# Performance work log

Measured on AMD Instinct MI355X. Metric: run time of the kernel, lower is better.

## Reference

```python
import jax, jax.numpy as jnp
import numpy as np
import math

D_PAIR = 64
N_HEADS = 4
D_HEAD = D_PAIR // N_HEADS


def setup_inputs() -> dict:
    key = jax.random.key(0)
    ks = jax.random.split(key, 9)
    B, L, D = 2, 256, D_PAIR
    s = 1.0 / math.sqrt(D)
    return {
        "z": jax.random.normal(ks[0], (B, L, L, D), dtype=jnp.float32),
        "ln_scale": jnp.ones((D,), jnp.float32),
        "ln_bias": jnp.zeros((D,), jnp.float32),
        "Wq": jax.random.normal(ks[1], (D, D), jnp.float32) * s,
        "Wk": jax.random.normal(ks[2], (D, D), jnp.float32) * s,
        "Wv": jax.random.normal(ks[3], (D, D), jnp.float32) * s,
        "Wg": jax.random.normal(ks[4], (D, D), jnp.float32) * s,
        "bg": jax.random.normal(ks[5], (D,), jnp.float32) * 0.02,
        "Wo": jax.random.normal(ks[6], (D, D), jnp.float32) * s,
        "bo": jax.random.normal(ks[7], (D,), jnp.float32) * 0.02,
    }


def _layernorm(x, scale, bias, eps=1e-5):
    mu = jnp.mean(x, axis=-1, keepdims=True)
    var = jnp.var(x, axis=-1, keepdims=True)
    return (x - mu) * jax.lax.rsqrt(var + eps) * scale + bias


def reference(z, ln_scale, ln_bias, Wq, Wk, Wv, Wg, bg, Wo, bo):
    B, L, _, D = z.shape
    H, Dh = N_HEADS, D_HEAD
    zn = _layernorm(z, ln_scale, ln_bias)
    # torch Linear(no bias): x @ W.T
    Q = (zn @ Wq.T).reshape(B, L, L, H, Dh)
    K = (zn @ Wk.T).reshape(B, L, L, H, Dh)
    V = (zn @ Wv.T).reshape(B, L, L, H, Dh)
    scale = 1.0 / math.sqrt(Dh)
    # row-wise attention: for each row l, attend over column index j
    attn = jnp.einsum("blihd,bljhd->blhij", Q, K) * scale  # [B,L,H,L,L]
    attn = jax.nn.softmax(attn, axis=-1)
    out = jnp.einsum("blhij,bljhd->blihd", attn, V).reshape(B, L, L, D)
    gate = jax.nn.sigmoid(zn @ Wg.T + bg)
    out = gate * out
    return out @ Wo.T + bo
```

## Files before the change

kernel.cpp:

```cpp
#include <hip/hip_runtime.h>
#include <math.h>


typedef __attribute__((ext_vector_type(4))) float f32x4;
typedef __attribute__((ext_vector_type(8))) short s16x8;

#define MFMA16(a, b, c) __builtin_amdgcn_mfma_f32_16x16x32_bf16((a), (b), (c), 0, 0, 0)

__device__ __forceinline__ short f2bf(float x) {
    union { float f; unsigned u; } v; v.f = x;
    unsigned r = v.u + 0x7fffu + ((v.u >> 16) & 1u);
    return (short)(r >> 16);
}
__device__ __forceinline__ s16x8 cvt8(const float* p) {
    s16x8 r;
    #pragma unroll
    for (int u = 0; u < 8; ++u) r[u] = f2bf(p[u]);
    return r;
}

static constexpr int VSTRIDE = 264;
static constexpr int PS = 40;

__global__ __launch_bounds__(256, 2)
void ka_fused(const float* __restrict__ z, const float* __restrict__ ln_s,
              const float* __restrict__ ln_b, const float* __restrict__ Wq,
              const float* __restrict__ Wk, const float* __restrict__ Wv,
              const float* __restrict__ Wg, const float* __restrict__ bg,
              short* __restrict__ ws)
{
    __shared__ __align__(16) short znl[256 * 64];
    __shared__ __align__(16) short Ksh[256 * 16];
    __shared__ __align__(16) short Vt[16 * VSTRIDE];
    __shared__ __align__(16) short rpb[4][64 * PS];

    const int tid = threadIdx.x, lane = tid & 63, w = tid >> 6;
    const int n16 = lane & 15, quad = lane >> 4;
    const bool qlo = (quad < 2);
    const int g = blockIdx.x, bl = g >> 2, h = g & 3;
    const size_t rowbase = (size_t)bl * (256 * 64);
    short* rp = rpb[w];

    {
        float zn[64];
        const float4* zp4 = (const float4*)(z + rowbase + (size_t)tid * 64);
        #pragma unroll
        for (int gq = 0; gq < 16; ++gq) {
            float4 v4 = zp4[gq];
            zn[gq * 4 + 0] = v4.x; zn[gq * 4 + 1] = v4.y;
            zn[gq * 4 + 2] = v4.z; zn[gq * 4 + 3] = v4.w;
        }
        float mu = 0.f;
        #pragma unroll
        for (int k = 0; k < 64; ++k) mu += zn[k];
        mu *= (1.f / 64.f);
        float va = 0.f;
        #pragma unroll
        for (int k = 0; k < 64; ++k) { float d = zn[k] - mu; va += d * d; }
        const float rs = rsqrtf(va * (1.f / 64.f) + 1e-5f);
        #pragma unroll
        for (int k = 0; k < 64; ++k) zn[k] = (zn[k] - mu) * rs * ln_s[k] + ln_b[k];
        #pragma unroll
        for (int gq = 0; gq < 8; ++gq) {
            s16x8 v;
            #pragma unroll
            for (int u = 0; u < 8; ++u) v[u] = f2bf(zn[gq * 8 + u]);
            *(s16x8*)&znl[tid * 64 + ((gq ^ (tid & 7)) * 8)] = v;
        }
    }

    s16x8 bfr[4][2];
    {
        const float* Wt0 = Wq; const float* Wt1 = Wk;
        const float* Wt2 = Wv; const float* Wt3 = Wg;
        #pragma unroll
        for (int ks = 0; ks < 2; ++ks) {
            size_t off = (size_t)(h * 16 + n16) * 64 + ks * 32 + quad * 8;
            bfr[0][ks] = cvt8(Wt0 + off);
            bfr[1][ks] = cvt8(Wt1 + off);
            bfr[2][ks] = cvt8(Wt2 + off);
            bfr[3][ks] = cvt8(Wt3 + off);
        }
    }
    const float bgv = bg[h * 16 + n16];

    f32x4 g4[4];
    #pragma unroll
    for (int mt = 0; mt < 4; ++mt) {
        const int row = w * 64 + mt * 16 + n16;
        s16x8 a0 = *(const s16x8*)&znl[row * 64 + ((quad ^ (n16 & 7)) * 8)];
        s16x8 a1 = *(const s16x8*)&znl[row * 64 + (((4 + quad) ^ (n16 & 7)) * 8)];
        f32x4 aq = {}, ak = {}, av = {}, ag = {};
        aq = MFMA16(a0, bfr[0][0], aq); aq = MFMA16(a1, bfr[0][1], aq);
        ak = MFMA16(a0, bfr[1][0], ak); ak = MFMA16(a1, bfr[1][1], ak);
        av = MFMA16(a0, bfr[2][0], av); av = MFMA16(a1, bfr[2][1], av);
        ag = MFMA16(a0, bfr[3][0], ag); ag = MFMA16(a1, bfr[3][1], ag);
        #pragma unroll
        for (int r = 0; r < 4; ++r)
            rp[(mt * 16 + quad * 4 + r) * PS + n16] = f2bf(0.25f * aq[r]);
        #pragma unroll
        for (int r = 0; r < 4; ++r) {
            int pos = w * 64 + mt * 16 + quad * 4 + r;
            Ksh[pos * 16 + (((n16 >> 3) ^ (pos & 1)) * 8) + (n16 & 7)] = f2bf(ak[r]);
        }
        {
            unsigned lo = (unsigned)(unsigned short)f2bf(av[0]) |
                          ((unsigned)(unsigned short)f2bf(av[1]) << 16);
            unsigned hi = (unsigned)(unsigned short)f2bf(av[2]) |
                          ((unsigned)(unsigned short)f2bf(av[3]) << 16);
            uint2 pk = {lo, hi};
            *(uint2*)&Vt[n16 * VSTRIDE + w * 64 + mt * 16 + quad * 4] = pk;
        }
        #pragma unroll
        for (int r = 0; r < 4; ++r)
            g4[mt][r] = 1.f / (1.f + __expf(-(ag[r] + bgv)));
    }

    s16x8 qa[4];
    #pragma unroll
    for (int mt = 0; mt < 4; ++mt) {
        s16x8 q = {};
        if (qlo) q = *(const s16x8*)&rp[(mt * 16 + n16) * PS + quad * 8];
        qa[mt] = q;
    }
    __syncthreads();

    float lrow[4][4];
    f32x4 o4[4];
    #pragma unroll
    for (int mt = 0; mt < 4; ++mt) {
        o4[mt] = {};
        #pragma unroll
        for (int r = 0; r < 4; ++r) lrow[mt][r] = 0.f;
    }
    for (int ch = 0; ch < 8; ++ch) {
        #pragma unroll
        for (int jtl = 0; jtl < 2; ++jtl) {
            int j = ch * 32 + jtl * 16 + n16;
            s16x8 kf = {};
            if (qlo) kf = *(const s16x8*)&Ksh[j * 16 + ((quad ^ (j & 1)) * 8)];
            int jc = jtl * 16 + n16, jb = jc >> 3;
            #pragma unroll
            for (int mt = 0; mt < 4; ++mt) {
                f32x4 zc = {};
                f32x4 s = MFMA16(qa[mt], kf, zc);
                #pragma unroll
                for (int r = 0; r < 4; ++r) {
                    float e = __expf(s[r]);
                    lrow[mt][r] += e;
                    int rin = mt * 16 + quad * 4 + r;
                    rp[rin * PS + ((jb ^ (rin & 3)) * 8) + (jc & 7)] = f2bf(e);
                }
            }
        }
        #pragma unroll
        for (int mt = 0; mt < 4; ++mt) {
            int rin = mt * 16 + n16;
            s16x8 pa = *(const s16x8*)&rp[rin * PS + ((quad ^ (rin & 3)) * 8)];
            s16x8 vf = *(const s16x8*)&Vt[n16 * VSTRIDE + ch * 32 + quad * 8];
            o4[mt] = MFMA16(pa, vf, o4[mt]);
        }
    }
    #pragma unroll
    for (int d = 1; d < 16; d <<= 1)
        #pragma unroll
        for (int mt = 0; mt < 4; ++mt)
            #pragma unroll
            for (int r = 0; r < 4; ++r)
                lrow[mt][r] += __shfl_xor(lrow[mt][r], d);

    #pragma unroll
    for (int mt = 0; mt < 4; ++mt)
        #pragma unroll
        for (int r = 0; r < 4; ++r) {
            float go = g4[mt][r] * o4[mt][r] / lrow[mt][r];
            rp[(mt * 16 + quad * 4 + r) * PS + n16] = f2bf(go);
        }
    {
        s16x8 p0 = *(const s16x8*)&rp[lane * PS];
        s16x8 p1 = *(const s16x8*)&rp[lane * PS + 8];
        short* dst = ws + (((size_t)h * 512 + bl) * 256 + w * 64 + lane) * 16;
        *(s16x8*)&dst[0] = p0;
        *(s16x8*)&dst[8] = p1;
    }
}

__global__ __launch_bounds__(256, 4)
void k3_out(const short* __restrict__ ws, const float* __restrict__ Wo,
            const float* __restrict__ bo, float* __restrict__ out)
{
    const int tid = threadIdx.x, lane = tid & 63, w = tid >> 6;
    const int n16 = lane & 15, quad = lane >> 4;
    const short* GO = ws;
    const int bl = blockIdx.x;
    const int rowloc = w * 64;

    s16x8 bfr[4][2];
    #pragma unroll
    for (int nt = 0; nt < 4; ++nt)
        #pragma unroll
        for (int ks = 0; ks < 2; ++ks)
            bfr[nt][ks] = cvt8(Wo + (size_t)(nt * 16 + n16) * 64 + ks * 32 + quad * 8);

    f32x4 acc[4][4] = {};
    #pragma unroll
    for (int mt = 0; mt < 4; ++mt) {
        #pragma unroll
        for (int c = 0; c < 2; ++c) {
            int hp = c * 2 + (quad >> 1);
            const short* ap = &GO[(((size_t)hp * 512 + bl) * 256 + rowloc + mt * 16 + n16) * 16
                                  + (quad & 1) * 8];
            s16x8 a = *(const s16x8*)ap;
            #pragma unroll
            for (int nt = 0; nt < 4; ++nt)
                acc[mt][nt] = MFMA16(a, bfr[nt][c], acc[mt][nt]);
        }
    }
    #pragma unroll
    for (int nt = 0; nt < 4; ++nt) {
        float bov = bo[nt * 16 + n16];
        #pragma unroll
        for (int mt = 0; mt < 4; ++mt)
            #pragma unroll
            for (int r = 0; r < 4; ++r)
                out[((size_t)bl * 256 + rowloc + mt * 16 + quad * 4 + r) * 64 + nt * 16 + n16] =
                    acc[mt][nt][r] + bov;
    }
}

extern "C" void kernel_launch(void* const* d_in, const int* in_sizes, int n_in,
                              void* d_out, int out_size, void* d_ws, size_t ws_size,
                              hipStream_t stream) {
    const float* z  = (const float*)d_in[0];
    const float* ls = (const float*)d_in[1];
    const float* lb = (const float*)d_in[2];
    const float* Wq = (const float*)d_in[3];
    const float* Wk = (const float*)d_in[4];
    const float* Wv = (const float*)d_in[5];
    const float* Wg = (const float*)d_in[6];
    const float* bg = (const float*)d_in[7];
    const float* Wo = (const float*)d_in[8];
    const float* bo = (const float*)d_in[9];
    float* out = (float*)d_out;
    short* wsp = (short*)d_ws;

    hipLaunchKernelGGL(ka_fused, dim3(2048), dim3(256), 0, stream,
                       z, ls, lb, Wq, Wk, Wv, Wg, bg, wsp);
    hipLaunchKernelGGL(k3_out, dim3(512), dim3(256), 0, stream, wsp, Wo, bo, out);
}
```

Baseline: 174.9 us.

## Alias attention LDS buffers, transpose MFMA operands, use exp2 and packed bf16 conversion

Shared memory is merged into one buffer. The per-wave probability and Q staging reuse the LayerNorm tile region, which cuts LDS per block so three blocks fit per CU instead of two. The Q/K/gate MFMAs are transposed so that scores come out in a key-major layout. That makes the row sum mostly a per-lane reduction needing two shuffles, and lets the P stores be packed 64-bit writes. Softmax uses exp2 with log2(e) folded into the Q scale, bf16 conversion uses the hardware packed intrinsic, and the output projection kernel runs twice as many smaller blocks. The risks are register pressure under the tighter launch bound and new bank-conflict patterns from the changed swizzles.

```diff
diff --git a/kernel.cpp b/kernel.cpp
--- a/kernel.cpp
+++ b/kernel.cpp
@@ -1,4 +1,5 @@
 #include <hip/hip_runtime.h>
+#include <hip/hip_bf16.h>
 #include <math.h>
 
 
@@ -7,39 +8,38 @@
 
 #define MFMA16(a, b, c) __builtin_amdgcn_mfma_f32_16x16x32_bf16((a), (b), (c), 0, 0, 0)
 
-__device__ __forceinline__ short f2bf(float x) {
-    union { float f; unsigned u; } v; v.f = x;
-    unsigned r = v.u + 0x7fffu + ((v.u >> 16) & 1u);
-    return (short)(r >> 16);
+__device__ __forceinline__ unsigned pk2(float a, float b) {
+    union { __hip_bfloat162 h; unsigned u; } c;
+    float2 t; t.x = a; t.y = b;
+    c.h = __float22bfloat162_rn(t);
+    return c.u;
 }
 __device__ __forceinline__ s16x8 cvt8(const float* p) {
-    s16x8 r;
-    #pragma unroll
-    for (int u = 0; u < 8; ++u) r[u] = f2bf(p[u]);
-    return r;
-}
-
-static constexpr int VSTRIDE = 264;
-static constexpr int PS = 40;
-
-__global__ __launch_bounds__(256, 2)
+    union { unsigned u[4]; s16x8 v; } r;
+    r.u[0] = pk2(p[0], p[1]); r.u[1] = pk2(p[2], p[3]);
+    r.u[2] = pk2(p[4], p[5]); r.u[3] = pk2(p[6], p[7]);
+    return r.v;
+}
+
+static constexpr int ZNL = 0;
+static constexpr int KSH = 16384;
+static constexpr int VT  = 20480;
+static constexpr int LDS_EL = 24704;
+
+__global__ __launch_bounds__(256, 3)
 void ka_fused(const float* __restrict__ z, const float* __restrict__ ln_s,
               const float* __restrict__ ln_b, const float* __restrict__ Wq,
               const float* __restrict__ Wk, const float* __restrict__ Wv,
               const float* __restrict__ Wg, const float* __restrict__ bg,
               short* __restrict__ ws)
 {
-    __shared__ __align__(16) short znl[256 * 64];
-    __shared__ __align__(16) short Ksh[256 * 16];
-    __shared__ __align__(16) short Vt[16 * VSTRIDE];
-    __shared__ __align__(16) short rpb[4][64 * PS];
-
+    __shared__ __align__(16) short lds[LDS_EL];
     const int tid = threadIdx.x, lane = tid & 63, w = tid >> 6;
     const int n16 = lane & 15, quad = lane >> 4;
     const bool qlo = (quad < 2);
     const int g = blockIdx.x, bl = g >> 2, h = g & 3;
     const size_t rowbase = (size_t)bl * (256 * 64);
-    short* rp = rpb[w];
+    const int wsl = w * 4096;
 
     {
         float zn[64];
@@ -60,128 +60,118 @@
         const float rs = rsqrtf(va * (1.f / 64.f) + 1e-5f);
         #pragma unroll
         for (int k = 0; k < 64; ++k) zn[k] = (zn[k] - mu) * rs * ln_s[k] + ln_b[k];
+        const int lr = lane;
         #pragma unroll
         for (int gq = 0; gq < 8; ++gq) {
-            s16x8 v;
-            #pragma unroll
-            for (int u = 0; u < 8; ++u) v[u] = f2bf(zn[gq * 8 + u]);
-            *(s16x8*)&znl[tid * 64 + ((gq ^ (tid & 7)) * 8)] = v;
-        }
-    }
-
-    s16x8 bfr[4][2];
-    {
-        const float* Wt0 = Wq; const float* Wt1 = Wk;
-        const float* Wt2 = Wv; const float* Wt3 = Wg;
-        #pragma unroll
-        for (int ks = 0; ks < 2; ++ks) {
-            size_t off = (size_t)(h * 16 + n16) * 64 + ks * 32 + quad * 8;
-            bfr[0][ks] = cvt8(Wt0 + off);
-            bfr[1][ks] = cvt8(Wt1 + off);
-            bfr[2][ks] = cvt8(Wt2 + off);
-            bfr[3][ks] = cvt8(Wt3 + off);
-        }
-    }
-    const float bgv = bg[h * 16 + n16];
-
-    f32x4 g4[4];
-    #pragma unroll
-    for (int mt = 0; mt < 4; ++mt) {
-        const int row = w * 64 + mt * 16 + n16;
-        s16x8 a0 = *(const s16x8*)&znl[row * 64 + ((quad ^ (n16 & 7)) * 8)];
-        s16x8 a1 = *(const s16x8*)&znl[row * 64 + (((4 + quad) ^ (n16 & 7)) * 8)];
+            union { unsigned u[4]; s16x8 v; } pkv;
+            pkv.u[0] = pk2(zn[gq * 8 + 0], zn[gq * 8 + 1]);
+            pkv.u[1] = pk2(zn[gq * 8 + 2], zn[gq * 8 + 3]);
+            pkv.u[2] = pk2(zn[gq * 8 + 4], zn[gq * 8 + 5]);
+            pkv.u[3] = pk2(zn[gq * 8 + 6], zn[gq * 8 + 7]);
+            *(s16x8*)&lds[ZNL + wsl + (lr >> 4) * 1024 + (lr & 15) * 64
+                          + ((gq ^ (lr & 7)) * 8)] = pkv.v;
+        }
+    }
+
+    s16x8 bq[2], bk[2], bv[2], bgf[2];
+    #pragma unroll
+    for (int ks = 0; ks < 2; ++ks) {
+        size_t off = (size_t)(h * 16 + n16) * 64 + ks * 32 + quad * 8;
+        bq[ks] = cvt8(Wq + off);  bk[ks] = cvt8(Wk + off);
+        bv[ks] = cvt8(Wv + off);  bgf[ks] = cvt8(Wg + off);
+    }
+    const float4 bg4 = *(const float4*)(bg + h * 16 + quad * 4);
+    constexpr float QS = 0.25f * 1.44269504088896340736f;
+
+    float g4t[4][4];
+    #pragma unroll
+    for (int t = 0; t < 4; ++t) {
+        s16x8 zn0 = *(const s16x8*)&lds[ZNL + wsl + t * 1024 + n16 * 64
+                                        + ((quad ^ (n16 & 7)) * 8)];
+        s16x8 zn1 = *(const s16x8*)&lds[ZNL + wsl + t * 1024 + n16 * 64
+                                        + (((4 + quad) ^ (n16 & 7)) * 8)];
         f32x4 aq = {}, ak = {}, av = {}, ag = {};
-        aq = MFMA16(a0, bfr[0][0], aq); aq = MFMA16(a1, bfr[0][1], aq);
-        ak = MFMA16(a0, bfr[1][0], ak); ak = MFMA16(a1, bfr[1][1], ak);
-        av = MFMA16(a0, bfr[2][0], av); av = MFMA16(a1, bfr[2][1], av);
-        ag = MFMA16(a0, bfr[3][0], ag); ag = MFMA16(a1, bfr[3][1], ag);
+        aq = MFMA16(bq[0], zn0, aq);  aq = MFMA16(bq[1], zn1, aq);
+        ak = MFMA16(bk[0], zn0, ak);  ak = MFMA16(bk[1], zn1, ak);
+        ag = MFMA16(bgf[0], zn0, ag); ag = MFMA16(bgf[1], zn1, ag);
+        av = MFMA16(zn0, bv[0], av);  av = MFMA16(zn1, bv[1], av);
+        {
+            uint2 p = {pk2(aq[0] * QS, aq[1] * QS), pk2(aq[2] * QS, aq[3] * QS)};
+            *(uint2*)&lds[ZNL + wsl + t * 1024 + n16 * 16 + quad * 4] = p;
+        }
+        {
+            uint2 p = {pk2(ak[0], ak[1]), pk2(ak[2], ak[3])};
+            *(uint2*)&lds[KSH + (w * 64 + t * 16 + n16) * 16 + quad * 4] = p;
+        }
+        {
+            uint2 p = {pk2(av[0], av[1]), pk2(av[2], av[3])};
+            *(uint2*)&lds[VT + n16 * 264 + (w * 64 + t * 16 + quad * 4)] = p;
+        }
         #pragma unroll
         for (int r = 0; r < 4; ++r)
-            rp[(mt * 16 + quad * 4 + r) * PS + n16] = f2bf(0.25f * aq[r]);
-        #pragma unroll
-        for (int r = 0; r < 4; ++r) {
-            int pos = w * 64 + mt * 16 + quad * 4 + r;
-            Ksh[pos * 16 + (((n16 >> 3) ^ (pos & 1)) * 8) + (n16 & 7)] = f2bf(ak[r]);
-        }
-        {
-            unsigned lo = (unsigned)(unsigned short)f2bf(av[0]) |
-                          ((unsigned)(unsigned short)f2bf(av[1]) << 16);
-            unsigned hi = (unsigned)(unsigned short)f2bf(av[2]) |
-                          ((unsigned)(unsigned short)f2bf(av[3]) << 16);
-            uint2 pk = {lo, hi};
-            *(uint2*)&Vt[n16 * VSTRIDE + w * 64 + mt * 16 + quad * 4] = pk;
-        }
-        #pragma unroll
-        for (int r = 0; r < 4; ++r)
-            g4[mt][r] = 1.f / (1.f + __expf(-(ag[r] + bgv)));
+            g4t[t][r] = 1.f / (1.f + __expf(-(ag[r] + bg4[r])));
     }
 
     s16x8 qa[4];
     #pragma unroll
-    for (int mt = 0; mt < 4; ++mt) {
+    for (int qt = 0; qt < 4; ++qt) {
         s16x8 q = {};
-        if (qlo) q = *(const s16x8*)&rp[(mt * 16 + n16) * PS + quad * 8];
-        qa[mt] = q;
+        if (qlo) q = *(const s16x8*)&lds[ZNL + wsl + qt * 1024 + n16 * 16 + quad * 8];
+        qa[qt] = q;
     }
     __syncthreads();
 
     float lrow[4][4];
     f32x4 o4[4];
     #pragma unroll
-    for (int mt = 0; mt < 4; ++mt) {
-        o4[mt] = {};
-        #pragma unroll
-        for (int r = 0; r < 4; ++r) lrow[mt][r] = 0.f;
-    }
+    for (int qt = 0; qt < 4; ++qt) {
+        o4[qt] = {};
+        #pragma unroll
+        for (int r = 0; r < 4; ++r) lrow[qt][r] = 0.f;
+    }
+    const int sw = (n16 ^ (n16 >> 2)) & 3;
     for (int ch = 0; ch < 8; ++ch) {
         #pragma unroll
         for (int jtl = 0; jtl < 2; ++jtl) {
-            int j = ch * 32 + jtl * 16 + n16;
+            int jt = ch * 2 + jtl;
             s16x8 kf = {};
-            if (qlo) kf = *(const s16x8*)&Ksh[j * 16 + ((quad ^ (j & 1)) * 8)];
-            int jc = jtl * 16 + n16, jb = jc >> 3;
+            if (qlo) kf = *(const s16x8*)&lds[KSH + (jt * 16 + n16) * 16 + quad * 8];
+            const int po = (((jtl * 2 + (quad >> 1)) ^ sw) * 8) + (quad & 1) * 4;
             #pragma unroll
-            for (int mt = 0; mt < 4; ++mt) {
+            for (int qt = 0; qt < 4; ++qt) {
                 f32x4 zc = {};
-                f32x4 s = MFMA16(qa[mt], kf, zc);
-                #pragma unroll
-                for (int r = 0; r < 4; ++r) {
-                    float e = __expf(s[r]);
-                    lrow[mt][r] += e;
-                    int rin = mt * 16 + quad * 4 + r;
-                    rp[rin * PS + ((jb ^ (rin & 3)) * 8) + (jc & 7)] = f2bf(e);
-                }
+                f32x4 s = MFMA16(kf, qa[qt], zc);
+                float e0 = exp2f(s[0]), e1 = exp2f(s[1]);
+                float e2 = exp2f(s[2]), e3 = exp2f(s[3]);
+                lrow[qt][0] += e0; lrow[qt][1] += e1;
+                lrow[qt][2] += e2; lrow[qt][3] += e3;
+                uint2 p = {pk2(e0, e1), pk2(e2, e3)};
+                *(uint2*)&lds[ZNL + wsl + qt * 1024 + 256 + n16 * 40 + po] = p;
             }
         }
-        #pragma unroll
-        for (int mt = 0; mt < 4; ++mt) {
-            int rin = mt * 16 + n16;
-            s16x8 pa = *(const s16x8*)&rp[rin * PS + ((quad ^ (rin & 3)) * 8)];
-            s16x8 vf = *(const s16x8*)&Vt[n16 * VSTRIDE + ch * 32 + quad * 8];
-            o4[mt] = MFMA16(pa, vf, o4[mt]);
-        }
-    }
-    #pragma unroll
-    for (int d = 1; d < 16; d <<= 1)
-        #pragma unroll
-        for (int mt = 0; mt < 4; ++mt)
-            #pragma unroll
-            for (int r = 0; r < 4; ++r)
-                lrow[mt][r] += __shfl_xor(lrow[mt][r], d);
-
-    #pragma unroll
-    for (int mt = 0; mt < 4; ++mt)
-        #pragma unroll
-        for (int r = 0; r < 4; ++r) {
-            float go = g4[mt][r] * o4[mt][r] / lrow[mt][r];
-            rp[(mt * 16 + quad * 4 + r) * PS + n16] = f2bf(go);
-        }
-    {
-        s16x8 p0 = *(const s16x8*)&rp[lane * PS];
-        s16x8 p1 = *(const s16x8*)&rp[lane * PS + 8];
-        short* dst = ws + (((size_t)h * 512 + bl) * 256 + w * 64 + lane) * 16;
-        *(s16x8*)&dst[0] = p0;
-        *(s16x8*)&dst[8] = p1;
+        s16x8 vf = *(const s16x8*)&lds[VT + n16 * 264 + ch * 32 + quad * 8];
+        #pragma unroll
+        for (int qt = 0; qt < 4; ++qt) {
+            s16x8 pf = *(const s16x8*)&lds[ZNL + wsl + qt * 1024 + 256 + n16 * 40
+                                           + ((quad ^ sw) * 8)];
+            o4[qt] = MFMA16(vf, pf, o4[qt]);
+        }
+    }
+
+    #pragma unroll
+    for (int qt = 0; qt < 4; ++qt) {
+        float l = lrow[qt][0] + lrow[qt][1] + lrow[qt][2] + lrow[qt][3];
+        l += __shfl_xor(l, 16);
+        l += __shfl_xor(l, 32);
+        const float inv = 1.f / l;
+        float g0 = g4t[qt][0] * o4[qt][0] * inv;
+        float g1 = g4t[qt][1] * o4[qt][1] * inv;
+        float g2 = g4t[qt][2] * o4[qt][2] * inv;
+        float g3 = g4t[qt][3] * o4[qt][3] * inv;
+        uint2 p = {pk2(g0, g1), pk2(g2, g3)};
+        short* dst = ws + (((size_t)h * 512 + bl) * 256 + w * 64 + qt * 16 + n16) * 16
+                     + quad * 4;
+        *(uint2*)dst = p;
     }
 }
 
@@ -192,8 +182,8 @@
     const int tid = threadIdx.x, lane = tid & 63, w = tid >> 6;
     const int n16 = lane & 15, quad = lane >> 4;
     const short* GO = ws;
-    const int bl = blockIdx.x;
-    const int rowloc = w * 64;
+    const int bl = blockIdx.x >> 1, half = blockIdx.x & 1;
+    const int rowloc = half * 128 + w * 32;
 
     s16x8 bfr[4][2];
     #pragma unroll
@@ -202,9 +192,9 @@
         for (int ks = 0; ks < 2; ++ks)
             bfr[nt][ks] = cvt8(Wo + (size_t)(nt * 16 + n16) * 64 + ks * 32 + quad * 8);
 
-    f32x4 acc[4][4] = {};
-    #pragma unroll
-    for (int mt = 0; mt < 4; ++mt) {
+    f32x4 acc[2][4] = {};
+    #pragma unroll
+    for (int mt = 0; mt < 2; ++mt) {
         #pragma unroll
         for (int c = 0; c < 2; ++c) {
             int hp = c * 2 + (quad >> 1);
@@ -220,7 +210,7 @@
     for (int nt = 0; nt < 4; ++nt) {
         float bov = bo[nt * 16 + n16];
         #pragma unroll
-        for (int mt = 0; mt < 4; ++mt)
+        for (int mt = 0; mt < 2; ++mt)
             #pragma unroll
             for (int r = 0; r < 4; ++r)
                 out[((size_t)bl * 256 + rowloc + mt * 16 + quad * 4 + r) * 64 + nt * 16 + n16] =
@@ -246,5 +236,5 @@
 
     hipLaunchKernelGGL(ka_fused, dim3(2048), dim3(256), 0, stream,
                        z, ls, lb, Wq, Wk, Wv, Wg, bg, wsp);
-    hipLaunchKernelGGL(k3_out, dim3(512), dim3(256), 0, stream, wsp, Wo, bo, out);
-}
+    hipLaunchKernelGGL(k3_out, dim3(1024), dim3(256), 0, stream, wsp, Wo, bo, out);
+}
```

Measured after the change: 174.5 us. Within noise of the previous version (-0.2%).
